# Kernel tuning notes

Hardware: AMD Instinct MI355X
Metric: run time of the kernel (lower is better)

## Reference

```python
import jax, jax.numpy as jnp
import numpy as np

# Module hyperparameters (from init_kwargs)
B = 8          # batch_size
NV = 8192      # num_template_vertices
NS = 4096      # num_fixed_samples
NPD = 64       # round(NS ** 0.5)
L_BOUND = 0.0
U_BOUND = 1.0
BD = (U_BOUND - L_BOUND) / (NPD - 1)   # min_sigma default
D_DIM = 2.0
C = (4.0 / (D_DIM + 2)) ** (1.0 / (D_DIM + 4)) * NV ** (-1.0 / (D_DIM + 4))
CF = (2.0 * np.pi) ** (-D_DIM / 2) / C ** D_DIM
CN = -1.0 / (2.0 * C ** 2)


def _make_grid():
    g = jnp.linspace(L_BOUND, U_BOUND, NPD, dtype=jnp.float32)
    gx, gy = jnp.meshgrid(g, g, indexing='ij')          # torch.meshgrid default 'ij'
    S = jnp.stack([gx, gy], axis=-1).reshape(NPD * NPD, 2)
    return jnp.broadcast_to(S[None], (B, NPD * NPD, 2))  # [B, npd^2, 2]


def setup_inputs() -> dict:
    key = jax.random.key(0)
    T = jax.random.uniform(key, (B, NV, 2), dtype=jnp.float32)  # UV in [0,1]
    S = _make_grid()
    return {"T": T, "S": S}


def reference(T, S):
    # sigma: per-batch bandwidth from vertex spread (torch std is unbiased, ddof=1)
    sigma = jnp.clip(jnp.std(T, axis=1, ddof=1).mean(axis=-1), BD)  # [B]
    # batched squared-L2 cdist: D[b,i,j] = ||S[b,i] - T[b,j]||^2  -> [B, npd^2, nV]
    s2 = jnp.sum(S * S, axis=-1)[:, :, None]
    t2 = jnp.sum(T * T, axis=-1)[:, None, :]
    cross = jnp.einsum('bik,bjk->bij', S, T)
    D = s2 + t2 - 2.0 * cross
    # Gaussian kernel density estimate at each grid point, mean over vertices
    E = jnp.exp(CN * D / (sigma[:, None, None] ** 2))
    K_H = CF * sigma[:, None] ** (-D_DIM) * E.mean(axis=-1)    # [B, npd^2]
    # normalize to a histogram
    return K_H / jnp.clip(K_H.sum(axis=1, keepdims=True), 1e-05)
```

## Files before the change

kernel.cpp:

```cpp
#include <hip/hip_runtime.h>
#include <math.h>

#define BATCH 8
#define NVERT 8192
#define NPD   64
#define NCELL 4096
#define SPLITS 64
#define JPB   (NVERT / SPLITS)
#define KR    32
#define ROUNDS (JPB / KR)

#ifndef M_PI
#define M_PI 3.14159265358979323846
#endif

#define TOTPART_OFF  0
#define PARAMS_OFF   1024
#define PARTIALS_OFF 4096

typedef __attribute__((ext_vector_type(8))) short  bf16x8;
typedef __attribute__((ext_vector_type(4))) float  f32x4;

static __device__ __forceinline__ float fast_exp2(float x) {
#if __has_builtin(__builtin_amdgcn_exp2f)
    return __builtin_amdgcn_exp2f(x);
#else
    return exp2f(x);
#endif
}

static __device__ __forceinline__ unsigned int pack_bf16(float a, float b) {
    unsigned int ua = __float_as_uint(a), ub = __float_as_uint(b);
    ua += 0x7fffu + ((ua >> 16) & 1u);
    ub += 0x7fffu + ((ub >> 16) & 1u);
    return (ua >> 16) | (ub & 0xffff0000u);
}

__global__ __launch_bounds__(256) void kde_kernel(const float* __restrict__ T,
                                                  float* __restrict__ params,
                                                  float* __restrict__ totpart,
                                                  float* __restrict__ partials) {
    const int b   = blockIdx.x >> 6;
    const int sp  = blockIdx.x & (SPLITS - 1);
    const int j0  = sp * JPB;
    const int tid = threadIdx.x;
    const int w    = tid >> 6;
    const int lane = tid & 63;

    __shared__ __align__(16) unsigned short exT[2][64][40];
    __shared__ __align__(16) unsigned short eyT[2][64][40];
    __shared__ float2 tj[JPB];
    __shared__ float  red[4][4];
    __shared__ float  bcast[2];

    const float4* T4 = reinterpret_cast<const float4*>(T + (size_t)b * NVERT * 2);
    float sx = 0.f, sx2 = 0.f, sy = 0.f, sy2 = 0.f;
    for (int q = tid; q < NVERT / 2; q += 256) {
        float4 v = T4[q];
        sx += v.x + v.z;
        sy += v.y + v.w;
        sx2 += v.x * v.x + v.z * v.z;
        sy2 += v.y * v.y + v.w * v.w;
        int local = 2 * q - j0;
        if ((unsigned)local < (unsigned)JPB)
            *reinterpret_cast<float4*>(&tj[local]) = v;
    }
    for (int off = 32; off; off >>= 1) {
        sx  += __shfl_down(sx,  off);  sx2 += __shfl_down(sx2, off);
        sy  += __shfl_down(sy,  off);  sy2 += __shfl_down(sy2, off);
    }
    if (lane == 0) { red[w][0] = sx; red[w][1] = sx2; red[w][2] = sy; red[w][3] = sy2; }
    __syncthreads();
    if (tid == 0) {
        double tsx = 0, tsx2 = 0, tsy = 0, tsy2 = 0;
        for (int i = 0; i < 4; ++i) {
            tsx += red[i][0]; tsx2 += red[i][1]; tsy += red[i][2]; tsy2 += red[i][3];
        }
        const double N = (double)NVERT;
        double varx = (tsx2 - tsx * tsx / N) / (N - 1.0);
        double vary = (tsy2 - tsy * tsy / N) / (N - 1.0);
        double sigma = 0.5 * (sqrt(varx) + sqrt(vary));
        const double BD = 1.0 / 63.0;
        if (sigma < BD) sigma = BD;
        const double C2 = pow(2.0, -13.0 / 3.0);
        double s2 = sigma * sigma;
        bcast[0] = (float)(-0.5 / C2 / (s2 * 0.69314718055994530942));
        bcast[1] = (float)(1.0 / (2.0 * M_PI * C2) / (s2 * N));
        if (sp == 0) params[b] = bcast[1];
    }
    __syncthreads();
    const float kexp2 = bcast[0];

    const float xg   = (float)lane * (1.0f / 63.0f);
    const int   jh   = (w >> 1) << 4;
    const bool  isY  = (w & 1);

#define STAGE(R, BUF)                                                       \
    {                                                                       \
        unsigned short (*dstT)[40] = isY ? eyT[BUF] : exT[BUF];             \
        _Pragma("unroll")                                                   \
        for (int jp = 0; jp < 8; ++jp) {                                    \
            int jl = jh + jp * 2;                                           \
            float4 tt = *reinterpret_cast<const float4*>(&tj[(R) * KR + jl]);\
            float tv0 = isY ? tt.y : tt.x;                                  \
            float tv1 = isY ? tt.w : tt.z;                                  \
            float d0 = xg - tv0, d1 = xg - tv1;                             \
            float e0 = fast_exp2(kexp2 * d0 * d0);                          \
            float e1 = fast_exp2(kexp2 * d1 * d1);                          \
            *reinterpret_cast<unsigned int*>(&dstT[lane][jl]) =             \
                pack_bf16(e0, e1);                                          \
        }                                                                   \
    }

    const int col16 = lane & 15;
    const int kq    = lane >> 4;
    f32x4 acc[4];
#pragma unroll
    for (int ni = 0; ni < 4; ++ni) acc[ni] = (f32x4){0.f, 0.f, 0.f, 0.f};

    STAGE(0, 0);
    for (int r = 0; r < ROUNDS; ++r) {
        __syncthreads();
        if (r + 1 < ROUNDS) STAGE(r + 1, (r + 1) & 1);
        const int buf = r & 1;
        bf16x8 af = *reinterpret_cast<const bf16x8*>(&exT[buf][(w << 4) + col16][kq << 3]);
#pragma unroll
        for (int ni = 0; ni < 4; ++ni) {
            bf16x8 bfr = *reinterpret_cast<const bf16x8*>(&eyT[buf][(ni << 4) + col16][kq << 3]);
            acc[ni] = __builtin_amdgcn_mfma_f32_16x16x32_bf16(af, bfr, acc[ni], 0, 0, 0);
        }
    }

    float* dst = partials + (size_t)blockIdx.x * NCELL;
    float tsum = 0.f;
    const int rowbase = (w << 4) + (kq << 2);
#pragma unroll
    for (int ni = 0; ni < 4; ++ni) {
#pragma unroll
        for (int r = 0; r < 4; ++r) {
            dst[(rowbase + r) * 64 + (ni << 4) + col16] = acc[ni][r];
            tsum += acc[ni][r];
        }
    }
    for (int off = 32; off; off >>= 1) tsum += __shfl_down(tsum, off);
    if (lane == 0) red[w][0] = tsum;
    __syncthreads();
    if (tid == 0)
        totpart[blockIdx.x] = (red[0][0] + red[1][0]) + (red[2][0] + red[3][0]);
}

__global__ __launch_bounds__(128) void finish_kernel(const float* __restrict__ partials,
                                                     const float* __restrict__ totpart,
                                                     const float* __restrict__ params,
                                                     float* __restrict__ out) {
    const int b     = blockIdx.x >> 5;
    const int strip = blockIdx.x & 31;
    const int cell  = strip * 128 + threadIdx.x;
    const float* p  = partials + (size_t)b * SPLITS * NCELL + cell;

    float s[8] = {0.f, 0.f, 0.f, 0.f, 0.f, 0.f, 0.f, 0.f};
#pragma unroll
    for (int k8 = 0; k8 < 8; ++k8)
#pragma unroll
        for (int j = 0; j < 8; ++j)
            s[j] += p[(size_t)(k8 * 8 + j) * NCELL];
    float sum = ((s[0] + s[1]) + (s[2] + s[3])) + ((s[4] + s[5]) + (s[6] + s[7]));

    __shared__ float tot_s;
    if (threadIdx.x < 64) {
        float v = totpart[b * SPLITS + threadIdx.x];
        for (int off = 32; off; off >>= 1) v += __shfl_down(v, off);
        if (threadIdx.x == 0) tot_s = v;
    }
    __syncthreads();

    const float scale = params[b];
    const float denom = fmaxf(tot_s * scale, 1e-5f);
    out[b * NCELL + cell] = (sum * scale) / denom;
}

extern "C" void kernel_launch(void* const* d_in, const int* in_sizes, int n_in,
                              void* d_out, int out_size, void* d_ws, size_t ws_size,
                              hipStream_t stream) {
    const float* T = (const float*)d_in[0];

    float* ws       = (float*)d_ws;
    float* totpart  = ws + TOTPART_OFF;
    float* params   = ws + PARAMS_OFF;
    float* partials = ws + PARTIALS_OFF;

    kde_kernel<<<BATCH * SPLITS, 256, 0, stream>>>(T, params, totpart, partials);
    finish_kernel<<<BATCH * 32, 128, 0, stream>>>(partials, totpart, params,
                                                  (float*)d_out);
}
```

Baseline: 69.47 us.

## Tile output grid per block and fuse normalization via last-block atomic counter

Replaces the vertex-split kernel, which wrote 64 partial grids per batch, plus a separate finish kernel with a single kernel. Each block owns a 16x16 output tile, and its four waves each handle a quarter of the vertices, so partials are reduced in shared memory instead of through global memory. The last block to finish for each batch, found with an atomic counter reset by a memset, normalizes the histogram in place. This removes the large partials traffic and one launch, but launches only 128 blocks, each looping serially over 64 rounds, and adds a memset.

Result: slower. 97.43 us (+40.2%).

```diff
diff --git a/kernel.cpp b/kernel.cpp
--- a/kernel.cpp
+++ b/kernel.cpp
@@ -1,22 +1,18 @@
 #include <hip/hip_runtime.h>
 #include <math.h>
 
-#define BATCH 8
-#define NVERT 8192
-#define NPD   64
-#define NCELL 4096
-#define SPLITS 64
-#define JPB   (NVERT / SPLITS)
-#define KR    32
-#define ROUNDS (JPB / KR)
+#define BATCH  8
+#define NVERT  8192
+#define NCELL  4096
+#define TPB    16
+#define KR     32
+#define KCH    (NVERT / 4)
+#define ROUNDS (KCH / KR)
+#define POISON 0xAAAAAAAAu
 
 #ifndef M_PI
 #define M_PI 3.14159265358979323846
 #endif
-
-#define TOTPART_OFF  0
-#define PARAMS_OFF   1024
-#define PARTIALS_OFF 4096
 
 typedef __attribute__((ext_vector_type(8))) short  bf16x8;
 typedef __attribute__((ext_vector_type(4))) float  f32x4;
@@ -36,22 +32,23 @@
     return (ua >> 16) | (ub & 0xffff0000u);
 }
 
-__global__ __launch_bounds__(256) void kde_kernel(const float* __restrict__ T,
-                                                  float* __restrict__ params,
-                                                  float* __restrict__ totpart,
-                                                  float* __restrict__ partials) {
-    const int b   = blockIdx.x >> 6;
-    const int sp  = blockIdx.x & (SPLITS - 1);
-    const int j0  = sp * JPB;
+__global__ __launch_bounds__(256) void kde_last(const float* __restrict__ T,
+                                                unsigned int* __restrict__ cnt,
+                                                float* __restrict__ out) {
+    const int blk = blockIdx.x;
+    const int b   = blk >> 4;
+    const int t   = blk & 15;
+    const int tr0 = (t >> 2) << 4;
+    const int tc0 = (t & 3) << 4;
     const int tid = threadIdx.x;
     const int w    = tid >> 6;
     const int lane = tid & 63;
 
-    __shared__ __align__(16) unsigned short exT[2][64][40];
-    __shared__ __align__(16) unsigned short eyT[2][64][40];
-    __shared__ float2 tj[JPB];
-    __shared__ float  red[4][4];
-    __shared__ float  bcast[2];
+    __shared__ __align__(16) unsigned short es[4][2][16][40];
+    __shared__ float red[4][4];
+    __shared__ float gsum[4][16][17];
+    __shared__ float bc[3];
+    __shared__ unsigned int lastflag;
 
     const float4* T4 = reinterpret_cast<const float4*>(T + (size_t)b * NVERT * 2);
     float sx = 0.f, sx2 = 0.f, sy = 0.f, sy2 = 0.f;
@@ -61,9 +58,6 @@
         sy += v.y + v.w;
         sx2 += v.x * v.x + v.z * v.z;
         sy2 += v.y * v.y + v.w * v.w;
-        int local = 2 * q - j0;
-        if ((unsigned)local < (unsigned)JPB)
-            *reinterpret_cast<float4*>(&tj[local]) = v;
     }
     for (int off = 32; off; off >>= 1) {
         sx  += __shfl_down(sx,  off);  sx2 += __shfl_down(sx2, off);
@@ -84,99 +78,91 @@
         if (sigma < BD) sigma = BD;
         const double C2 = pow(2.0, -13.0 / 3.0);
         double s2 = sigma * sigma;
-        bcast[0] = (float)(-0.5 / C2 / (s2 * 0.69314718055994530942));
-        bcast[1] = (float)(1.0 / (2.0 * M_PI * C2) / (s2 * N));
-        if (sp == 0) params[b] = bcast[1];
+        bc[0] = (float)(-0.5 / C2 / (s2 * 0.69314718055994530942));
+        bc[1] = (float)(1.0 / (2.0 * M_PI * C2) / (s2 * N));
     }
     __syncthreads();
-    const float kexp2 = bcast[0];
+    const float kexp2 = bc[0];
 
-    const float xg   = (float)lane * (1.0f / 63.0f);
-    const int   jh   = (w >> 1) << 4;
-    const bool  isY  = (w & 1);
-
-#define STAGE(R, BUF)                                                       \
-    {                                                                       \
-        unsigned short (*dstT)[40] = isY ? eyT[BUF] : exT[BUF];             \
-        _Pragma("unroll")                                                   \
-        for (int jp = 0; jp < 8; ++jp) {                                    \
-            int jl = jh + jp * 2;                                           \
-            float4 tt = *reinterpret_cast<const float4*>(&tj[(R) * KR + jl]);\
-            float tv0 = isY ? tt.y : tt.x;                                  \
-            float tv1 = isY ? tt.w : tt.z;                                  \
-            float d0 = xg - tv0, d1 = xg - tv1;                             \
-            float e0 = fast_exp2(kexp2 * d0 * d0);                          \
-            float e1 = fast_exp2(kexp2 * d1 * d1);                          \
-            *reinterpret_cast<unsigned int*>(&dstT[lane][jl]) =             \
-                pack_bf16(e0, e1);                                          \
-        }                                                                   \
+    const int   vp    = lane & 15;
+    const int   plane = lane >> 5;
+    const int   rb    = ((lane >> 4) & 1) * 8;
+    const int   base0 = plane ? tc0 : tr0;
+    float c1[8], m2[8];
+#pragma unroll
+    for (int i = 0; i < 8; ++i) {
+        float xg = (float)(base0 + rb + i) * (1.0f / 63.0f);
+        m2[i] = -2.0f * kexp2 * xg;
+        c1[i] = kexp2 * xg * xg;
     }
 
-    const int col16 = lane & 15;
-    const int kq    = lane >> 4;
-    f32x4 acc[4];
+    unsigned short (*exw)[40] = es[w][0];
+    unsigned short (*eyw)[40] = es[w][1];
+    unsigned short (*dstT)[40] = es[w][plane];
+    const float4* T4v = reinterpret_cast<const float4*>(T) + (size_t)b * 4096 + w * 1024;
+
+    const int frow = lane & 15;
+    const int kq   = lane >> 4;
+    f32x4 acc = (f32x4){0.f, 0.f, 0.f, 0.f};
+
+    for (int r = 0; r < ROUNDS; ++r) {
+        float4 tt = T4v[r * 16 + vp];
+        float t0 = plane ? tt.y : tt.x;
+        float t1 = plane ? tt.w : tt.z;
+        float kt20 = kexp2 * t0 * t0;
+        float kt21 = kexp2 * t1 * t1;
 #pragma unroll
-    for (int ni = 0; ni < 4; ++ni) acc[ni] = (f32x4){0.f, 0.f, 0.f, 0.f};
-
-    STAGE(0, 0);
-    for (int r = 0; r < ROUNDS; ++r) {
-        __syncthreads();
-        if (r + 1 < ROUNDS) STAGE(r + 1, (r + 1) & 1);
-        const int buf = r & 1;
-        bf16x8 af = *reinterpret_cast<const bf16x8*>(&exT[buf][(w << 4) + col16][kq << 3]);
-#pragma unroll
-        for (int ni = 0; ni < 4; ++ni) {
-            bf16x8 bfr = *reinterpret_cast<const bf16x8*>(&eyT[buf][(ni << 4) + col16][kq << 3]);
-            acc[ni] = __builtin_amdgcn_mfma_f32_16x16x32_bf16(af, bfr, acc[ni], 0, 0, 0);
+        for (int i = 0; i < 8; ++i) {
+            float e0 = fast_exp2(fmaf(m2[i], t0, c1[i] + kt20));
+            float e1 = fast_exp2(fmaf(m2[i], t1, c1[i] + kt21));
+            *reinterpret_cast<unsigned int*>(&dstT[rb + i][vp * 2]) = pack_bf16(e0, e1);
         }
+        bf16x8 af = *reinterpret_cast<const bf16x8*>(&exw[frow][kq << 3]);
+        bf16x8 bf = *reinterpret_cast<const bf16x8*>(&eyw[frow][kq << 3]);
+        acc = __builtin_amdgcn_mfma_f32_16x16x32_bf16(af, bf, acc, 0, 0, 0);
     }
 
-    float* dst = partials + (size_t)blockIdx.x * NCELL;
-    float tsum = 0.f;
-    const int rowbase = (w << 4) + (kq << 2);
 #pragma unroll
-    for (int ni = 0; ni < 4; ++ni) {
-#pragma unroll
-        for (int r = 0; r < 4; ++r) {
-            dst[(rowbase + r) * 64 + (ni << 4) + col16] = acc[ni][r];
-            tsum += acc[ni][r];
-        }
-    }
-    for (int off = 32; off; off >>= 1) tsum += __shfl_down(tsum, off);
-    if (lane == 0) red[w][0] = tsum;
+    for (int ri = 0; ri < 4; ++ri)
+        gsum[w][(kq << 2) + ri][frow] = acc[ri];
     __syncthreads();
-    if (tid == 0)
-        totpart[blockIdx.x] = (red[0][0] + red[1][0]) + (red[2][0] + red[3][0]);
-}
+    const int rr = tid >> 4, cc = tid & 15;
+    const float raw = (gsum[0][rr][cc] + gsum[1][rr][cc])
+                    + (gsum[2][rr][cc] + gsum[3][rr][cc]);
+    out[b * NCELL + (tr0 + rr) * 64 + tc0 + cc] = raw;
 
-__global__ __launch_bounds__(128) void finish_kernel(const float* __restrict__ partials,
-                                                     const float* __restrict__ totpart,
-                                                     const float* __restrict__ params,
-                                                     float* __restrict__ out) {
-    const int b     = blockIdx.x >> 5;
-    const int strip = blockIdx.x & 31;
-    const int cell  = strip * 128 + threadIdx.x;
-    const float* p  = partials + (size_t)b * SPLITS * NCELL + cell;
-
-    float s[8] = {0.f, 0.f, 0.f, 0.f, 0.f, 0.f, 0.f, 0.f};
-#pragma unroll
-    for (int k8 = 0; k8 < 8; ++k8)
-#pragma unroll
-        for (int j = 0; j < 8; ++j)
-            s[j] += p[(size_t)(k8 * 8 + j) * NCELL];
-    float sum = ((s[0] + s[1]) + (s[2] + s[3])) + ((s[4] + s[5]) + (s[6] + s[7]));
-
-    __shared__ float tot_s;
-    if (threadIdx.x < 64) {
-        float v = totpart[b * SPLITS + threadIdx.x];
-        for (int off = 32; off; off >>= 1) v += __shfl_down(v, off);
-        if (threadIdx.x == 0) tot_s = v;
+    __threadfence();
+    __syncthreads();
+    if (tid == 0) {
+        unsigned int old = atomicAdd(&cnt[b], 1u);
+        lastflag = (old == 15u || old == POISON + 15u) ? 1u : 0u;
     }
     __syncthreads();
+    if (!lastflag) return;
 
-    const float scale = params[b];
-    const float denom = fmaxf(tot_s * scale, 1e-5f);
-    out[b * NCELL + cell] = (sum * scale) / denom;
+    __threadfence();
+    float* ob = out + b * NCELL;
+    float v[16];
+    float s = 0.f;
+#pragma unroll
+    for (int i = 0; i < 16; ++i) {
+        v[i] = ob[i * 256 + tid];
+        s += v[i];
+    }
+    for (int off = 32; off; off >>= 1) s += __shfl_down(s, off);
+    if (lane == 0) red[w][0] = s;
+    __syncthreads();
+    if (tid == 0) {
+        const float tot   = (red[0][0] + red[1][0]) + (red[2][0] + red[3][0]);
+        const float scale = bc[1];
+        const float denom = fmaxf(tot * scale, 1e-5f);
+        bc[2] = scale / denom;
+    }
+    __syncthreads();
+    const float factor = bc[2];
+#pragma unroll
+    for (int i = 0; i < 16; ++i)
+        ob[i * 256 + tid] = v[i] * factor;
 }
 
 extern "C" void kernel_launch(void* const* d_in, const int* in_sizes, int n_in,
@@ -184,12 +170,7 @@
                               hipStream_t stream) {
     const float* T = (const float*)d_in[0];
 
-    float* ws       = (float*)d_ws;
-    float* totpart  = ws + TOTPART_OFF;
-    float* params   = ws + PARAMS_OFF;
-    float* partials = ws + PARTIALS_OFF;
-
-    kde_kernel<<<BATCH * SPLITS, 256, 0, stream>>>(T, params, totpart, partials);
-    finish_kernel<<<BATCH * 32, 128, 0, stream>>>(partials, totpart, params,
-                                                  (float*)d_out);
+    unsigned int* cnt = (unsigned int*)d_ws;
+    hipMemsetAsync(cnt, 0, BATCH * sizeof(unsigned int), stream);
+    kde_last<<<BATCH * TPB, 256, 0, stream>>>(T, cnt, (float*)d_out);
 }
```
